# Performance work log

Measured on AMD Instinct MI355X. Metric: run time of the kernel, lower is better.

Reference implementation:

```python
import jax, jax.numpy as jnp
import numpy as np

IN_BIAS = 5.0   # self.input_bias
W_BIAS = 5.0    # self.weight_bias
ALPHA = 1.0     # LnExp_Max smooth-max temperature
MIN_VAL = 1e-12 # Ln clamp (module constructs Ln(min_val=1e-12))
STRIDE = 1


def extract_patches(x, fh, fw, stride):
    """TF-style extract_image_patches: (N,C,H,W) -> (N, fh*fw*C, oh, ow)
    with patch elements ordered (kh, kw, C) to match k.view(fh*fw*in_c, oc)
    flattening of a (fh, fw, in_c, oc) kernel."""
    N, C, H, W = x.shape
    oh = (H - fh) // stride + 1
    ow = (W - fw) // stride + 1
    tiles = [x[:, :, i:i + (oh - 1) * stride + 1:stride,
                    j:j + (ow - 1) * stride + 1:stride]
             for i in range(fh) for j in range(fw)]  # fh*fw slices (small fixed loop)
    p = jnp.stack(tiles, axis=1)  # (N, fh*fw, C, oh, ow)
    return p.reshape(N, fh * fw * C, oh, ow)


def setup_inputs() -> dict:
    key = jax.random.key(0)
    k1, k2 = jax.random.split(key)
    N, C, H, W = 8, 16, 32, 32
    FH, FW, OC = 3, 3, 64
    x = jax.random.normal(k1, (N, C, H, W), dtype=jnp.float32)
    # xavier-uniform-ish init for kernel (fh, fw, in_c, oc)
    fan_in = FH * FW * C
    fan_out = FH * FW * OC
    limit = float(np.sqrt(6.0 / (fan_in + fan_out)))
    k = jax.random.uniform(k2, (FH, FW, C, OC), dtype=jnp.float32,
                           minval=-limit, maxval=limit)
    bias = jnp.zeros((OC,), dtype=jnp.float32)
    delta_x = jnp.asarray(1.0, dtype=jnp.float32)
    delta_w = jnp.asarray(1.0, dtype=jnp.float32)
    return {"x": x, "k": k, "bias": bias, "delta_x": delta_x, "delta_w": delta_w}


def reference(x, k, bias, delta_x, delta_w):
    fh, fw, cin, oc = k.shape
    # Ln(x + input_bias)
    ln_x = jnp.log(jnp.maximum(x + IN_BIAS, MIN_VAL))
    p_ln = extract_patches(ln_x, fh, fw, STRIDE)          # (N, P, oh, ow)
    p_raw = extract_patches(x, fh, fw, STRIDE)            # (N, P, oh, ow)
    p_ln = p_ln[:, :, None, :, :]                         # (N, P, 1, oh, ow)
    k_flat = k.reshape(fh * fw * cin, oc)                 # (P, OC)
    # broadcast add in log domain -> huge intermediate (N, P, OC, oh, ow)
    x1_k1 = p_ln + (k_flat + W_BIAS)[None, :, :, None, None]
    # LnExp_Max (smooth max via scaled logsumexp over patch dim) then Exp
    y11 = jnp.exp(jax.nn.logsumexp(ALPHA * x1_k1, axis=1) / ALPHA)  # (N, OC, oh, ow)
    # bias corrections
    x_sum = jnp.sum(p_raw, axis=1, keepdims=True) * delta_w          # (N, 1, oh, ow)
    k_sum = (jnp.sum(k_flat, axis=0) * delta_x)[None, :, None, None] # (1, OC, 1, 1)
    return y11 - x_sum - k_sum + bias[None, :, None, None]
```

## Files before the change

kernel.cpp:

```cpp
#include <hip/hip_runtime.h>

#define NN 8
#define CC 16
#define HH 32
#define WW 32
#define OCH 64
#define OH 30
#define OW 30

__global__ __launch_bounds__(256) void bm_smax_kernel(
    const float* __restrict__ x, const float* __restrict__ kw_,
    const float* __restrict__ bias, const float* __restrict__ pdx,
    const float* __restrict__ pdw, float* __restrict__ out)
{
    __shared__ __align__(16) float sE[144 * OCH];
    __shared__ float sA[3 * WW * 17];
    __shared__ float sKsum[OCH];
    __shared__ float sRaw[32];

    const int t = threadIdx.x;
    const int b = blockIdx.x;
    const int n = b / OH;
    const int y = b % OH;

    for (int idx = t; idx < 3 * CC * WW; idx += 256) {
        int w    = idx & 31;
        int rest = idx >> 5;
        int c    = rest & 15;
        int kh   = rest >> 4;
        float v = x[((n * CC + c) * HH + (y + kh)) * WW + w];
        sA[(kh * WW + w) * 17 + c] = fmaxf(v + 5.0f, 1e-12f);
    }
    for (int idx = t; idx < 144 * OCH; idx += 256) {
        sE[idx] = __expf(kw_[idx] + 5.0f);
    }
    if (t < 64) {
        float s = 0.f;
        for (int i = 0; i < 144; ++i) s += kw_[i * OCH + t];
        sKsum[t] = s * pdx[0];
    } else if (t < 96) {
        int xo = t - 64;
        float s = 0.f;
        if (xo < OW) {
            for (int kh = 0; kh < 3; ++kh)
                for (int c = 0; c < CC; ++c) {
                    const float* p = &x[((n * CC + c) * HH + (y + kh)) * WW + xo];
                    s += p[0] + p[1] + p[2];
                }
        }
        if (xo < 32) sRaw[xo] = s * pdw[0];
    }
    __syncthreads();

    const int xo  = t & 31;
    const int ocg = t >> 5;
    if (xo >= OW) return;

    float acc[8];
#pragma unroll
    for (int j = 0; j < 8; ++j) acc[j] = 0.f;

#pragma unroll
    for (int kh = 0; kh < 3; ++kh) {
#pragma unroll
        for (int kwi = 0; kwi < 3; ++kwi) {
            const int arow = (kh * WW + xo + kwi) * 17;
            const int erow = ((kh * 3 + kwi) * CC) * OCH + ocg * 8;
#pragma unroll
            for (int c = 0; c < CC; ++c) {
                float a = sA[arow + c];
                const float4 e0 = *(const float4*)&sE[erow + c * OCH];
                const float4 e1 = *(const float4*)&sE[erow + c * OCH + 4];
                acc[0] = fmaf(a, e0.x, acc[0]);
                acc[1] = fmaf(a, e0.y, acc[1]);
                acc[2] = fmaf(a, e0.z, acc[2]);
                acc[3] = fmaf(a, e0.w, acc[3]);
                acc[4] = fmaf(a, e1.x, acc[4]);
                acc[5] = fmaf(a, e1.y, acc[5]);
                acc[6] = fmaf(a, e1.z, acc[6]);
                acc[7] = fmaf(a, e1.w, acc[7]);
            }
        }
    }

    const float rsum = sRaw[xo];
#pragma unroll
    for (int j = 0; j < 8; ++j) {
        int oc = ocg * 8 + j;
        out[((n * OCH + oc) * OH + y) * OW + xo] = acc[j] - rsum - sKsum[oc] + bias[oc];
    }
}

extern "C" void kernel_launch(void* const* d_in, const int* in_sizes, int n_in,
                              void* d_out, int out_size, void* d_ws, size_t ws_size,
                              hipStream_t stream) {
    const float* x    = (const float*)d_in[0];
    const float* k    = (const float*)d_in[1];
    const float* bias = (const float*)d_in[2];
    const float* pdx  = (const float*)d_in[3];
    const float* pdw  = (const float*)d_in[4];
    float* out = (float*)d_out;

    bm_smax_kernel<<<NN * OH, 256, 0, stream>>>(x, k, bias, pdx, pdw, out);
}
```

Baseline: 79.83 us.

## Precompute exp(weights) in a prep kernel and register-tile main kernel 4x4

Moves the exp of the kernel weights and the bias/ksum coefficient into a separate prep kernel that writes to workspace. Each of the 240 main blocks then copies the precomputed table with float4 loads instead of recomputing 9216 exps. The main kernel drops to 128 threads, each computing a 4-output-column by 4-channel tile, so loaded activations are reused across the three kernel-width offsets. The cost is an extra kernel launch and a changed shared-memory layout.

```diff
diff --git a/kernel.cpp b/kernel.cpp
--- a/kernel.cpp
+++ b/kernel.cpp
@@ -7,87 +7,107 @@
 #define OCH 64
 #define OH 30
 #define OW 30
+#define KTOT 144
 
-__global__ __launch_bounds__(256) void bm_smax_kernel(
-    const float* __restrict__ x, const float* __restrict__ kw_,
-    const float* __restrict__ bias, const float* __restrict__ pdx,
+__global__ __launch_bounds__(256) void prep_kernel(
+    const float* __restrict__ kw_, const float* __restrict__ bias,
+    const float* __restrict__ pdx, float* __restrict__ ws)
+{
+    const int b = blockIdx.x, t = threadIdx.x;
+    if (b < 36) {
+        const int idx = b * 256 + t;
+        ws[idx] = __expf(kw_[idx] + 5.0f);
+    } else if (t < OCH) {
+        float s = 0.f;
+#pragma unroll 8
+        for (int i = 0; i < KTOT; ++i) s += kw_[i * OCH + t];
+        ws[9216 + t] = bias[t] - pdx[0] * s;
+    }
+}
+
+__global__ __launch_bounds__(128) void bm_main_kernel(
+    const float* __restrict__ x, const float* __restrict__ ws,
     const float* __restrict__ pdw, float* __restrict__ out)
 {
-    __shared__ __align__(16) float sE[144 * OCH];
-    __shared__ float sA[3 * WW * 17];
-    __shared__ float sKsum[OCH];
-    __shared__ float sRaw[32];
+    __shared__ __align__(16) float sE[KTOT * OCH];
+    __shared__ __align__(16) float sA[3 * CC * 36];
+    __shared__ float sRawDW[32];
+    __shared__ float sCoef[OCH];
 
     const int t = threadIdx.x;
-    const int b = blockIdx.x;
-    const int n = b / OH;
-    const int y = b % OH;
+    const int n = blockIdx.x / OH;
+    const int y = blockIdx.x % OH;
 
-    for (int idx = t; idx < 3 * CC * WW; idx += 256) {
-        int w    = idx & 31;
-        int rest = idx >> 5;
-        int c    = rest & 15;
-        int kh   = rest >> 4;
-        float v = x[((n * CC + c) * HH + (y + kh)) * WW + w];
-        sA[(kh * WW + w) * 17 + c] = fmaxf(v + 5.0f, 1e-12f);
+    {
+        const float4* __restrict__ src = (const float4*)ws;
+        float4* dst = (float4*)sE;
+        for (int i = t; i < KTOT * OCH / 4; i += 128) dst[i] = src[i];
     }
-    for (int idx = t; idx < 144 * OCH; idx += 256) {
-        sE[idx] = __expf(kw_[idx] + 5.0f);
+    for (int idx = t; idx < 3 * CC * WW; idx += 128) {
+        const int w = idx & 31;
+        const int rest = idx >> 5;
+        const float v = x[(((n * CC) + (rest & 15)) * HH + (y + (rest >> 4))) * WW + w];
+        sA[rest * 36 + w] = fmaxf(v + 5.0f, 1e-12f);
     }
-    if (t < 64) {
+    for (int idx = t; idx < 3 * CC * 4; idx += 128)
+        sA[(idx >> 2) * 36 + 32 + (idx & 3)] = 0.f;
+    if (t < OCH) sCoef[t] = ws[9216 + t];
+    if (t < 32) {
         float s = 0.f;
-        for (int i = 0; i < 144; ++i) s += kw_[i * OCH + t];
-        sKsum[t] = s * pdx[0];
-    } else if (t < 96) {
-        int xo = t - 64;
-        float s = 0.f;
-        if (xo < OW) {
+        if (t < OW) {
             for (int kh = 0; kh < 3; ++kh)
+#pragma unroll
                 for (int c = 0; c < CC; ++c) {
-                    const float* p = &x[((n * CC + c) * HH + (y + kh)) * WW + xo];
+                    const float* p = &x[((n * CC + c) * HH + (y + kh)) * WW + t];
                     s += p[0] + p[1] + p[2];
                 }
         }
-        if (xo < 32) sRaw[xo] = s * pdw[0];
+        sRawDW[t] = s * pdw[0];
     }
     __syncthreads();
 
-    const int xo  = t & 31;
-    const int ocg = t >> 5;
-    if (xo >= OW) return;
+    const int q  = t & 7;
+    const int og = t >> 3;
 
-    float acc[8];
+    float acc[4][4];
 #pragma unroll
-    for (int j = 0; j < 8; ++j) acc[j] = 0.f;
+    for (int xi = 0; xi < 4; ++xi)
+#pragma unroll
+        for (int j = 0; j < 4; ++j) acc[xi][j] = 0.f;
 
 #pragma unroll
     for (int kh = 0; kh < 3; ++kh) {
+#pragma unroll 4
+        for (int c = 0; c < CC; ++c) {
+            const float* arow = &sA[(kh * CC + c) * 36 + 4 * q];
+            const float4 a0 = *(const float4*)arow;
+            const float2 a1 = *(const float2*)(arow + 4);
+            const float a[6] = {a0.x, a0.y, a0.z, a0.w, a1.x, a1.y};
 #pragma unroll
-        for (int kwi = 0; kwi < 3; ++kwi) {
-            const int arow = (kh * WW + xo + kwi) * 17;
-            const int erow = ((kh * 3 + kwi) * CC) * OCH + ocg * 8;
+            for (int kwi = 0; kwi < 3; ++kwi) {
+                const float4 e = *(const float4*)&sE[((kh * 3 + kwi) * CC + c) * OCH + 4 * og];
 #pragma unroll
-            for (int c = 0; c < CC; ++c) {
-                float a = sA[arow + c];
-                const float4 e0 = *(const float4*)&sE[erow + c * OCH];
-                const float4 e1 = *(const float4*)&sE[erow + c * OCH + 4];
-                acc[0] = fmaf(a, e0.x, acc[0]);
-                acc[1] = fmaf(a, e0.y, acc[1]);
-                acc[2] = fmaf(a, e0.z, acc[2]);
-                acc[3] = fmaf(a, e0.w, acc[3]);
-                acc[4] = fmaf(a, e1.x, acc[4]);
-                acc[5] = fmaf(a, e1.y, acc[5]);
-                acc[6] = fmaf(a, e1.z, acc[6]);
-                acc[7] = fmaf(a, e1.w, acc[7]);
+                for (int xi = 0; xi < 4; ++xi) {
+                    const float av = a[xi + kwi];
+                    acc[xi][0] = fmaf(av, e.x, acc[xi][0]);
+                    acc[xi][1] = fmaf(av, e.y, acc[xi][1]);
+                    acc[xi][2] = fmaf(av, e.z, acc[xi][2]);
+                    acc[xi][3] = fmaf(av, e.w, acc[xi][3]);
+                }
             }
         }
     }
 
-    const float rsum = sRaw[xo];
 #pragma unroll
-    for (int j = 0; j < 8; ++j) {
-        int oc = ocg * 8 + j;
-        out[((n * OCH + oc) * OH + y) * OW + xo] = acc[j] - rsum - sKsum[oc] + bias[oc];
+    for (int xi = 0; xi < 4; ++xi) {
+        const int xo = 4 * q + xi;
+        if (xo < OW) {
+#pragma unroll
+            for (int j = 0; j < 4; ++j) {
+                const int oc = 4 * og + j;
+                out[((n * OCH + oc) * OH + y) * OW + xo] = acc[xi][j] - sRawDW[xo] + sCoef[oc];
+            }
+        }
     }
 }
 
@@ -100,6 +120,8 @@
     const float* pdx  = (const float*)d_in[3];
     const float* pdw  = (const float*)d_in[4];
     float* out = (float*)d_out;
+    float* ws  = (float*)d_ws;
 
-    bm_smax_kernel<<<NN * OH, 256, 0, stream>>>(x, k, bias, pdx, pdw, out);
+    prep_kernel<<<37, 256, 0, stream>>>(k, bias, pdx, ws);
+    bm_main_kernel<<<NN * OH, 128, 0, stream>>>(x, ws, pdw, out);
 }
```

Measured after the change: 81.50 us. +2.1%, slower.
